# Kernel tuning notes

Hardware: AMD Instinct MI355X
Metric: run time of the kernel (lower is better)

Reference implementation:

```python
import jax, jax.numpy as jnp
import numpy as np

KH, KW = 7, 7            # extraction kernel
EH, EW = 5, 5            # effective (cropped) kernel
PAD = (KH - EH) // 2     # = 1
EPS = 1e-7


def _extract_patches(x):
    # x: [B,H,W,C] -> patches [B,Ho,Wo,KH,KW,C], stride 1, VALID padding
    B, H, Wd, C = x.shape
    Ho, Wo = H - KH + 1, Wd - KW + 1
    rows = []
    for i in range(KH):
        cols = [x[:, i:i + Ho, j:j + Wo, :] for j in range(KW)]
        rows.append(jnp.stack(cols, axis=3))          # [B,Ho,Wo,KW,C]
    return jnp.stack(rows, axis=3)                     # [B,Ho,Wo,KH,KW,C]


def _rotate_bilinear(patches, angles):
    # patches: [N,KH,KW,C]; angles: [N]. Mirrors tf.contrib.image
    # angles_to_projective_transforms + transform(BILINEAR, fill=0).
    # Note: the layer's det(matrix)==0 NEAREST fallback never fires (det==1).
    N = patches.shape[0]
    c, s = jnp.cos(angles), jnp.sin(angles)
    Wm1, Hm1 = jnp.float32(KW - 1), jnp.float32(KH - 1)
    xo = (Wm1 - (c * Wm1 - s * Hm1)) * 0.5
    yo = (Hm1 - (s * Wm1 + c * Hm1)) * 0.5
    scale = jnp.float32(1.0 + EPS)   # transforms /= transforms[:,8:9]+1e-7
    a0, a1, a2 = c / scale, -s / scale, xo / scale
    a3, a4, a5 = s / scale, c / scale, yo / scale
    yg, xg = jnp.meshgrid(jnp.arange(KH, dtype=jnp.float32),
                          jnp.arange(KW, dtype=jnp.float32), indexing='ij')
    x_in = a0[:, None, None] * xg + a1[:, None, None] * yg + a2[:, None, None]
    y_in = a3[:, None, None] * xg + a4[:, None, None] * yg + a5[:, None, None]
    x0f = jnp.floor(x_in); y0f = jnp.floor(y_in)
    wx1 = x_in - x0f; wx0 = 1.0 - wx1
    wy1 = y_in - y0f; wy0 = 1.0 - wy1
    x0 = x0f.astype(jnp.int32); x1 = x0 + 1
    y0 = y0f.astype(jnp.int32); y1 = y0 + 1
    nidx = jnp.arange(N)[:, None, None]

    def corner(yi, xi, w):
        valid = ((xi >= 0) & (xi < KW) & (yi >= 0) & (yi < KH)).astype(patches.dtype)
        v = patches[nidx, jnp.clip(yi, 0, KH - 1), jnp.clip(xi, 0, KW - 1)]
        return (w * valid)[..., None] * v

    return (corner(y0, x0, wy0 * wx0) + corner(y0, x1, wy0 * wx1) +
            corner(y1, x0, wy1 * wx0) + corner(y1, x1, wy1 * wx1))


def reference(x, W, b):
    B, H, Wd, C = x.shape
    patches = _extract_patches(x)                      # [B,Ho,Wo,KH,KW,C]
    _, Ho, Wo = patches.shape[:3]
    intensity = jnp.sum(patches, axis=-1)              # [B,Ho,Wo,KH,KW]
    row_idx = jnp.repeat(jnp.arange(KH, dtype=jnp.float32), KW)   # rowMulti
    col_idx = jnp.tile(jnp.arange(KW, dtype=jnp.float32), KH)     # colMulti
    flat = intensity.reshape(-1, KH * KW)              # [N, KH*KW]
    denom = jnp.sum(flat, -1) + EPS
    cr = jnp.sum(flat * row_idx, -1) / denom - (KH - 1) / 2.0
    cc = jnp.sum(flat * col_idx, -1) / denom - (KW - 1) / 2.0
    angle = jnp.arctan2(cr, cc + EPS)                  # [N]
    patches_n = patches.reshape(-1, KH, KW, C)         # [N,KH,KW,C]
    rot = _rotate_bilinear(patches_n, angle)
    rot = rot[:, PAD:PAD + EH, PAD:PAD + EW, :]        # crop to effective
    rot = rot.reshape(B, Ho, Wo, EH * EW * C)
    w_flat = W.reshape(W.shape[0], -1)                 # [F, EH*EW*C]
    out = jnp.einsum('bhwk,fk->bhwf', rot, w_flat) + b
    return out


def setup_inputs() -> dict:
    key = jax.random.key(0)
    kx, kw, _ = jax.random.split(key, 3)
    x = jax.random.normal(kx, (8, 64, 64, 32), dtype=jnp.float32)
    W = jax.random.normal(kw, (64, EH, EW, 32), dtype=jnp.float32) * 0.05
    b = jnp.zeros((64,), dtype=jnp.float32)
    return {"x": x, "W": W, "b": b}
```

## Files before the change

kernel.cpp:

```cpp
#include <hip/hip_runtime.h>
#include <hip/hip_bf16.h>

#define EPSF 1e-7f
#define B_ 8
#define H_ 64
#define W_ 64
#define C_ 32
#define HO 58
#define WO 58
#define NF 64
#define KDIM 800

#define XBS 40

typedef __bf16 v8bf __attribute__((ext_vector_type(8)));
typedef float  v4f  __attribute__((ext_vector_type(4)));
typedef float  v2f  __attribute__((ext_vector_type(2)));

__global__ void k_wpack(const float* __restrict__ W, __bf16* __restrict__ Wp) {
    int t = blockIdx.x*256 + threadIdx.x;
    int j = t & 7; int lane = (t >> 3) & 63; int rest = t >> 9;
    int kb = rest % 25; int nt = rest / 25;
    int f = nt*16 + (lane & 15);
    int k = kb*32 + (lane >> 4)*8 + j;
    Wp[t] = (__bf16)W[f*KDIM + k];
}

__global__ __launch_bounds__(256, 4)
void k_main(const float* __restrict__ x, const v8bf* __restrict__ Wp,
            const float* __restrict__ bias, float* __restrict__ out) {
    __shared__ __bf16 xtb[8][22][XBS];
    __shared__ float  Srow[8][22];
    __shared__ float4 pars[32];
    __shared__ float  redu[2][64][20];

    int tid = threadIdx.x;
    int wv = tid >> 6, lane = tid & 63;
    int m = lane & 15, q = lane >> 4;
    int rh = wv & 1, kh = wv >> 1;

    int L = blockIdx.x + 4*(blockIdx.y + 29*blockIdx.z);
    int newL = (L & 7)*116 + (L >> 3);
    int b   = newL / 116;
    int rem = newL - b*116;
    int rg  = rem >> 2;
    int cg  = rem & 3;
    int ho0 = rg*2, wo0 = cg*16;
    int npx = WO - wo0; if (npx > 16) npx = 16;

    if (tid < 176) {
        int r = tid / 22, c = tid - r*22;
        int xc = wo0 + c; if (xc > W_-1) xc = W_-1;
        const float* src = x + (size_t)((b*H_ + ho0 + r)*W_ + xc)*C_;
        float4 vq[8];
#pragma unroll
        for (int qq = 0; qq < 8; qq++) vq[qq] = *(const float4*)(src + qq*4);
        float s = 0.f;
#pragma unroll
        for (int qq = 0; qq < 8; qq++) s += vq[qq].x + vq[qq].y + vq[qq].z + vq[qq].w;
        Srow[r][c] = s;
#pragma unroll
        for (int h8 = 0; h8 < 4; h8++) {
            v8bf o;
            o[0]=(__bf16)vq[h8*2].x;   o[1]=(__bf16)vq[h8*2].y;
            o[2]=(__bf16)vq[h8*2].z;   o[3]=(__bf16)vq[h8*2].w;
            o[4]=(__bf16)vq[h8*2+1].x; o[5]=(__bf16)vq[h8*2+1].y;
            o[6]=(__bf16)vq[h8*2+1].z; o[7]=(__bf16)vq[h8*2+1].w;
            *(v8bf*)&xtb[r][c][h8*8] = o;
        }
    }
    __syncthreads();

    if (tid < 32) {
        int r0 = tid >> 4, c0 = tid & 15;
        float den = 0.f, crn = 0.f, ccn = 0.f;
#pragma unroll
        for (int i = 0; i < 7; i++)
#pragma unroll
            for (int j = 0; j < 7; j++) {
                float v = Srow[r0 + i][c0 + j];
                den += v; crn += v*(float)i; ccn += v*(float)j;
            }
        float dt = den + EPSF;
        float cr = crn/dt - 3.0f;
        float cx = ccn/dt - 3.0f + EPSF;
        float r2 = cr*cr + cx*cx;
        float inv = r2 > 0.f ? rsqrtf(r2) : 0.f;
        float c_ = r2 > 0.f ? cx*inv : 1.0f;
        float s_ = cr*inv;
        const float scale = 1.0f + EPSF;
        float pc  = c_/scale, ps = s_/scale;
        float pxo = (6.0f - (c_*6.0f - s_*6.0f))*0.5f/scale;
        float pyo = (6.0f - (s_*6.0f + c_*6.0f))*0.5f/scale;
        pars[tid] = make_float4(pc, ps, pxo, pyo);
    }
    __syncthreads();

    float4 pp = pars[(rh << 4) | m];
    float pc = pp.x, ps = pp.y, pxo = pp.z, pyo = pp.w;

    const v8bf* wp = Wp + lane;
    const __bf16* patch = &xtb[rh][m][q*8];

    v4f acc0 = {0.f,0.f,0.f,0.f}, acc1 = {0.f,0.f,0.f,0.f};
    v4f acc2 = {0.f,0.f,0.f,0.f}, acc3 = {0.f,0.f,0.f,0.f};

    int kb0 = kh*13;
    int nkb = 13 - kh;
    int kblast = kb0 + nkb - 1;

    auto loadw = [&](v8bf* dst, int kbi) {
        dst[0] = wp[(0*25 + kbi)*64];
        dst[1] = wp[(1*25 + kbi)*64];
        dst[2] = wp[(2*25 + kbi)*64];
        dst[3] = wp[(3*25 + kbi)*64];
    };

    auto body = [&](int kb, const v8bf* wf) {
        unsigned ukb = (unsigned)kb;
        int py = (int)(ukb/5u);
        int pxx = kb - py*5;
        float yy = (float)(py + 1);
        float xx = (float)(pxx + 1);

        float xin = pc*xx - ps*yy + pxo;
        float yin = ps*xx + pc*yy + pyo;
        float x0f = floorf(xin), y0f = floorf(yin);
        float wx1 = xin - x0f, wx0 = 1.0f - wx1;
        float wy1 = yin - y0f, wy0 = 1.0f - wy1;
        int ix0 = (int)x0f, iy0 = (int)y0f;
        int ix1 = ix0 + 1,  iy1 = iy0 + 1;

        v2f a8[4];
#pragma unroll
        for (int d = 0; d < 4; d++) a8[d] = (v2f){0.f, 0.f};

        auto corner = [&](int yi, int xi, float wgt) {
            bool valid = (xi >= 0) & (xi < 7) & (yi >= 0) & (yi < 7);
            int cy  = yi < 0 ? 0 : (yi > 6 ? 6 : yi);
            int cx2 = xi < 0 ? 0 : (xi > 6 ? 6 : xi);
            float wq = valid ? wgt : 0.0f;
            union { v8bf v; unsigned u[4]; } uv;
            uv.v = *(const v8bf*)(patch + (cy*22 + cx2)*XBS);
            v2f w2 = (v2f){wq, wq};
#pragma unroll
            for (int d = 0; d < 4; d++) {
                v2f val = (v2f){ __uint_as_float(uv.u[d] << 16),
                                 __uint_as_float(uv.u[d] & 0xffff0000u) };
                a8[d] += w2 * val;
            }
        };
        corner(iy0, ix0, wy0*wx0);
        corner(iy0, ix1, wy0*wx1);
        corner(iy1, ix0, wy1*wx0);
        corner(iy1, ix1, wy1*wx1);

        v8bf af;
#pragma unroll
        for (int d = 0; d < 4; d++) {
            af[2*d]   = (__bf16)a8[d].x;
            af[2*d+1] = (__bf16)a8[d].y;
        }
        acc0 = __builtin_amdgcn_mfma_f32_16x16x32_bf16(af, wf[0], acc0, 0, 0, 0);
        acc1 = __builtin_amdgcn_mfma_f32_16x16x32_bf16(af, wf[1], acc1, 0, 0, 0);
        acc2 = __builtin_amdgcn_mfma_f32_16x16x32_bf16(af, wf[2], acc2, 0, 0, 0);
        acc3 = __builtin_amdgcn_mfma_f32_16x16x32_bf16(af, wf[3], acc3, 0, 0, 0);
    };

    v8bf wfA[4], wfB[4];
    loadw(wfA, kb0);
    int i = 0;
#pragma unroll 1
    for (; i + 2 <= nkb; i += 2) {
        loadw(wfB, kb0 + i + 1);
        body(kb0 + i, wfA);
        int nx = kb0 + i + 2; if (nx > kblast) nx = kblast;
        loadw(wfA, nx);
        body(kb0 + i + 1, wfB);
    }
    if (i < nkb) body(kblast, wfA);

    if (kh == 1) {
        *(v4f*)&redu[rh][lane][0]  = acc0;
        *(v4f*)&redu[rh][lane][4]  = acc1;
        *(v4f*)&redu[rh][lane][8]  = acc2;
        *(v4f*)&redu[rh][lane][12] = acc3;
    }
    __syncthreads();
    if (kh == 0) {
        acc0 += *(const v4f*)&redu[rh][lane][0];
        acc1 += *(const v4f*)&redu[rh][lane][4];
        acc2 += *(const v4f*)&redu[rh][lane][8];
        acc3 += *(const v4f*)&redu[rh][lane][12];

        float bv0 = bias[m], bv1 = bias[16 + m];
        float bv2 = bias[32 + m], bv3 = bias[48 + m];

        int ho = ho0 + rh;
        size_t rowbase = (size_t)(b*HO + ho)*WO + wo0;
#pragma unroll
        for (int r = 0; r < 4; r++) {
            int px = q*4 + r;
            if (px < npx) {
                float* op = out + (rowbase + px)*NF + m;
                op[0]  = acc0[r] + bv0;
                op[16] = acc1[r] + bv1;
                op[32] = acc2[r] + bv2;
                op[48] = acc3[r] + bv3;
            }
        }
    }
}

extern "C" void kernel_launch(void* const* d_in, const int* in_sizes, int n_in,
                              void* d_out, int out_size, void* d_ws, size_t ws_size,
                              hipStream_t stream) {
    const float* x    = (const float*)d_in[0];
    const float* W    = (const float*)d_in[1];
    const float* bias = (const float*)d_in[2];
    float* out = (float*)d_out;
    __bf16* Wp = (__bf16*)d_ws;

    k_wpack<<<dim3(200), 256, 0, stream>>>(W, Wp);
    k_main<<<dim3(4, 29, B_), 256, 0, stream>>>(x, (const v8bf*)Wp, bias, out);
}
```

Before: 76.83 us.

## Split K reduction across four waves per row with 512-thread blocks

Doubles the block to 512 threads so each pixel row's 25 K-blocks are split over four waves (7/6/6/6) instead of two, and reduces the three partial accumulators through shared memory. The weight-fragment double-buffering is dropped in favour of a simple loop that loads weights just before the MFMAs. The aim is more waves in flight and a shorter per-wave serial chain. In exchange it adds reduction traffic and raises launch bounds to 512x8, which may squeeze registers and expose global-load latency now that weights are no longer prefetched.

Measured after the change: 76.53 us. No clear change (-0.4%).

```diff
diff --git a/kernel.cpp b/kernel.cpp
--- a/kernel.cpp
+++ b/kernel.cpp
@@ -26,13 +26,13 @@
     Wp[t] = (__bf16)W[f*KDIM + k];
 }
 
-__global__ __launch_bounds__(256, 4)
+__global__ __launch_bounds__(512, 8)
 void k_main(const float* __restrict__ x, const v8bf* __restrict__ Wp,
             const float* __restrict__ bias, float* __restrict__ out) {
     __shared__ __bf16 xtb[8][22][XBS];
     __shared__ float  Srow[8][22];
     __shared__ float4 pars[32];
-    __shared__ float  redu[2][64][20];
+    __shared__ float  redu[3][2][64][16];
 
     int tid = threadIdx.x;
     int wv = tid >> 6, lane = tid & 63;
@@ -105,18 +105,12 @@
     v4f acc0 = {0.f,0.f,0.f,0.f}, acc1 = {0.f,0.f,0.f,0.f};
     v4f acc2 = {0.f,0.f,0.f,0.f}, acc3 = {0.f,0.f,0.f,0.f};
 
-    int kb0 = kh*13;
-    int nkb = 13 - kh;
+    int kb0 = (kh == 0) ? 0 : (7 + (kh - 1)*6);
+    int nkb = (kh == 0) ? 7 : 6;
     int kblast = kb0 + nkb - 1;
 
-    auto loadw = [&](v8bf* dst, int kbi) {
-        dst[0] = wp[(0*25 + kbi)*64];
-        dst[1] = wp[(1*25 + kbi)*64];
-        dst[2] = wp[(2*25 + kbi)*64];
-        dst[3] = wp[(3*25 + kbi)*64];
-    };
-
-    auto body = [&](int kb, const v8bf* wf) {
+#pragma unroll 1
+    for (int kb = kb0; kb <= kblast; kb++) {
         unsigned ukb = (unsigned)kb;
         int py = (int)(ukb/5u);
         int pxx = kb - py*5;
@@ -161,37 +155,34 @@
             af[2*d]   = (__bf16)a8[d].x;
             af[2*d+1] = (__bf16)a8[d].y;
         }
-        acc0 = __builtin_amdgcn_mfma_f32_16x16x32_bf16(af, wf[0], acc0, 0, 0, 0);
-        acc1 = __builtin_amdgcn_mfma_f32_16x16x32_bf16(af, wf[1], acc1, 0, 0, 0);
-        acc2 = __builtin_amdgcn_mfma_f32_16x16x32_bf16(af, wf[2], acc2, 0, 0, 0);
-        acc3 = __builtin_amdgcn_mfma_f32_16x16x32_bf16(af, wf[3], acc3, 0, 0, 0);
-    };
-
-    v8bf wfA[4], wfB[4];
-    loadw(wfA, kb0);
-    int i = 0;
-#pragma unroll 1
-    for (; i + 2 <= nkb; i += 2) {
-        loadw(wfB, kb0 + i + 1);
-        body(kb0 + i, wfA);
-        int nx = kb0 + i + 2; if (nx > kblast) nx = kblast;
-        loadw(wfA, nx);
-        body(kb0 + i + 1, wfB);
-    }
-    if (i < nkb) body(kblast, wfA);
-
-    if (kh == 1) {
-        *(v4f*)&redu[rh][lane][0]  = acc0;
-        *(v4f*)&redu[rh][lane][4]  = acc1;
-        *(v4f*)&redu[rh][lane][8]  = acc2;
-        *(v4f*)&redu[rh][lane][12] = acc3;
+
+        v8bf wf0 = wp[(0*25 + kb)*64];
+        v8bf wf1 = wp[(1*25 + kb)*64];
+        v8bf wf2 = wp[(2*25 + kb)*64];
+        v8bf wf3 = wp[(3*25 + kb)*64];
+
+        acc0 = __builtin_amdgcn_mfma_f32_16x16x32_bf16(af, wf0, acc0, 0, 0, 0);
+        acc1 = __builtin_amdgcn_mfma_f32_16x16x32_bf16(af, wf1, acc1, 0, 0, 0);
+        acc2 = __builtin_amdgcn_mfma_f32_16x16x32_bf16(af, wf2, acc2, 0, 0, 0);
+        acc3 = __builtin_amdgcn_mfma_f32_16x16x32_bf16(af, wf3, acc3, 0, 0, 0);
+    }
+
+    if (kh != 0) {
+        int p = kh - 1;
+        *(v4f*)&redu[p][rh][lane][0]  = acc0;
+        *(v4f*)&redu[p][rh][lane][4]  = acc1;
+        *(v4f*)&redu[p][rh][lane][8]  = acc2;
+        *(v4f*)&redu[p][rh][lane][12] = acc3;
     }
     __syncthreads();
     if (kh == 0) {
-        acc0 += *(const v4f*)&redu[rh][lane][0];
-        acc1 += *(const v4f*)&redu[rh][lane][4];
-        acc2 += *(const v4f*)&redu[rh][lane][8];
-        acc3 += *(const v4f*)&redu[rh][lane][12];
+#pragma unroll
+        for (int p = 0; p < 3; p++) {
+            acc0 += *(const v4f*)&redu[p][rh][lane][0];
+            acc1 += *(const v4f*)&redu[p][rh][lane][4];
+            acc2 += *(const v4f*)&redu[p][rh][lane][8];
+            acc3 += *(const v4f*)&redu[p][rh][lane][12];
+        }
 
         float bv0 = bias[m], bv1 = bias[16 + m];
         float bv2 = bias[32 + m], bv3 = bias[48 + m];
@@ -222,5 +213,5 @@
     __bf16* Wp = (__bf16*)d_ws;
 
     k_wpack<<<dim3(200), 256, 0, stream>>>(W, Wp);
-    k_main<<<dim3(4, 29, B_), 256, 0, stream>>>(x, (const v8bf*)Wp, bias, out);
+    k_main<<<dim3(4, 29, B_), 512, 0, stream>>>(x, (const v8bf*)Wp, bias, out);
 }
```

## Process eight output rows per block with two rows per wave sharing weights

Applied to the files above, without the earlier changes.

Each block now covers 8 output rows instead of 2, using 512 threads. Each wave handles two rows and reuses each loaded weight fragment for both rows' MFMAs. This cuts redundant global weight loads and the halo re-staging of the input tile, and shrinks the grid from 928 to 256 blocks. The last row group overlaps earlier rows (ho0=50), so some rows are computed and written twice with identical values. The risk is higher register pressure and a small grid of 256 blocks, which may leave compute units underused.

Result: no change. 75.77 us (-1.4%).

```diff
diff --git a/kernel.cpp b/kernel.cpp
--- a/kernel.cpp
+++ b/kernel.cpp
@@ -26,29 +26,30 @@
     Wp[t] = (__bf16)W[f*KDIM + k];
 }
 
-__global__ __launch_bounds__(256, 4)
+__global__ __launch_bounds__(512, 2)
 void k_main(const float* __restrict__ x, const v8bf* __restrict__ Wp,
             const float* __restrict__ bias, float* __restrict__ out) {
-    __shared__ __bf16 xtb[8][22][XBS];
-    __shared__ float  Srow[8][22];
-    __shared__ float4 pars[32];
-    __shared__ float  redu[2][64][20];
+    __shared__ __bf16 xtb[14][22][XBS];
+    __shared__ float  Srow[14][22];
+    __shared__ float4 pars[128];
+    __shared__ float  redu[2][4][64][20];
 
     int tid = threadIdx.x;
     int wv = tid >> 6, lane = tid & 63;
     int m = lane & 15, q = lane >> 4;
-    int rh = wv & 1, kh = wv >> 1;
-
-    int L = blockIdx.x + 4*(blockIdx.y + 29*blockIdx.z);
-    int newL = (L & 7)*116 + (L >> 3);
-    int b   = newL / 116;
-    int rem = newL - b*116;
+    int rp = wv & 3, kh = wv >> 2;
+
+    int L = blockIdx.x + 4*(blockIdx.y + 8*blockIdx.z);
+    int newL = (L & 7)*32 + (L >> 3);
+    int b   = newL >> 5;
+    int rem = newL & 31;
     int rg  = rem >> 2;
     int cg  = rem & 3;
-    int ho0 = rg*2, wo0 = cg*16;
+    int ho0 = (rg < 7) ? rg*8 : 50;
+    int wo0 = cg*16;
     int npx = WO - wo0; if (npx > 16) npx = 16;
 
-    if (tid < 176) {
+    if (tid < 308) {
         int r = tid / 22, c = tid - r*22;
         int xc = wo0 + c; if (xc > W_-1) xc = W_-1;
         const float* src = x + (size_t)((b*H_ + ho0 + r)*W_ + xc)*C_;
@@ -71,7 +72,7 @@
     }
     __syncthreads();
 
-    if (tid < 32) {
+    if (tid < 128) {
         int r0 = tid >> 4, c0 = tid & 15;
         float den = 0.f, crn = 0.f, ccn = 0.f;
 #pragma unroll
@@ -96,14 +97,18 @@
     }
     __syncthreads();
 
-    float4 pp = pars[(rh << 4) | m];
-    float pc = pp.x, ps = pp.y, pxo = pp.z, pyo = pp.w;
+    int rA = 2*rp, rB = 2*rp + 1;
+    float4 ppA = pars[(rA << 4) | m];
+    float4 ppB = pars[(rB << 4) | m];
 
     const v8bf* wp = Wp + lane;
-    const __bf16* patch = &xtb[rh][m][q*8];
-
-    v4f acc0 = {0.f,0.f,0.f,0.f}, acc1 = {0.f,0.f,0.f,0.f};
-    v4f acc2 = {0.f,0.f,0.f,0.f}, acc3 = {0.f,0.f,0.f,0.f};
+    const __bf16* patchA = &xtb[rA][m][q*8];
+    const __bf16* patchB = &xtb[rB][m][q*8];
+
+    v4f aA0 = {0.f,0.f,0.f,0.f}, aA1 = {0.f,0.f,0.f,0.f};
+    v4f aA2 = {0.f,0.f,0.f,0.f}, aA3 = {0.f,0.f,0.f,0.f};
+    v4f aB0 = {0.f,0.f,0.f,0.f}, aB1 = {0.f,0.f,0.f,0.f};
+    v4f aB2 = {0.f,0.f,0.f,0.f}, aB3 = {0.f,0.f,0.f,0.f};
 
     int kb0 = kh*13;
     int nkb = 13 - kh;
@@ -116,7 +121,9 @@
         dst[3] = wp[(3*25 + kbi)*64];
     };
 
-    auto body = [&](int kb, const v8bf* wf) {
+    auto bodyhalf = [&](int kb, const v8bf* wf, const __bf16* patch,
+                        float pc, float ps, float pxo, float pyo,
+                        v4f& A0, v4f& A1, v4f& A2, v4f& A3) {
         unsigned ukb = (unsigned)kb;
         int py = (int)(ukb/5u);
         int pxx = kb - py*5;
@@ -161,10 +168,15 @@
             af[2*d]   = (__bf16)a8[d].x;
             af[2*d+1] = (__bf16)a8[d].y;
         }
-        acc0 = __builtin_amdgcn_mfma_f32_16x16x32_bf16(af, wf[0], acc0, 0, 0, 0);
-        acc1 = __builtin_amdgcn_mfma_f32_16x16x32_bf16(af, wf[1], acc1, 0, 0, 0);
-        acc2 = __builtin_amdgcn_mfma_f32_16x16x32_bf16(af, wf[2], acc2, 0, 0, 0);
-        acc3 = __builtin_amdgcn_mfma_f32_16x16x32_bf16(af, wf[3], acc3, 0, 0, 0);
+        A0 = __builtin_amdgcn_mfma_f32_16x16x32_bf16(af, wf[0], A0, 0, 0, 0);
+        A1 = __builtin_amdgcn_mfma_f32_16x16x32_bf16(af, wf[1], A1, 0, 0, 0);
+        A2 = __builtin_amdgcn_mfma_f32_16x16x32_bf16(af, wf[2], A2, 0, 0, 0);
+        A3 = __builtin_amdgcn_mfma_f32_16x16x32_bf16(af, wf[3], A3, 0, 0, 0);
+    };
+
+    auto body = [&](int kb, const v8bf* wf) {
+        bodyhalf(kb, wf, patchA, ppA.x, ppA.y, ppA.z, ppA.w, aA0, aA1, aA2, aA3);
+        bodyhalf(kb, wf, patchB, ppB.x, ppB.y, ppB.z, ppB.w, aB0, aB1, aB2, aB3);
     };
 
     v8bf wfA[4], wfB[4];
@@ -181,32 +193,47 @@
     if (i < nkb) body(kblast, wfA);
 
     if (kh == 1) {
-        *(v4f*)&redu[rh][lane][0]  = acc0;
-        *(v4f*)&redu[rh][lane][4]  = acc1;
-        *(v4f*)&redu[rh][lane][8]  = acc2;
-        *(v4f*)&redu[rh][lane][12] = acc3;
+        *(v4f*)&redu[0][rp][lane][0]  = aA0;
+        *(v4f*)&redu[0][rp][lane][4]  = aA1;
+        *(v4f*)&redu[0][rp][lane][8]  = aA2;
+        *(v4f*)&redu[0][rp][lane][12] = aA3;
+        *(v4f*)&redu[1][rp][lane][0]  = aB0;
+        *(v4f*)&redu[1][rp][lane][4]  = aB1;
+        *(v4f*)&redu[1][rp][lane][8]  = aB2;
+        *(v4f*)&redu[1][rp][lane][12] = aB3;
     }
     __syncthreads();
     if (kh == 0) {
-        acc0 += *(const v4f*)&redu[rh][lane][0];
-        acc1 += *(const v4f*)&redu[rh][lane][4];
-        acc2 += *(const v4f*)&redu[rh][lane][8];
-        acc3 += *(const v4f*)&redu[rh][lane][12];
+        aA0 += *(const v4f*)&redu[0][rp][lane][0];
+        aA1 += *(const v4f*)&redu[0][rp][lane][4];
+        aA2 += *(const v4f*)&redu[0][rp][lane][8];
+        aA3 += *(const v4f*)&redu[0][rp][lane][12];
+        aB0 += *(const v4f*)&redu[1][rp][lane][0];
+        aB1 += *(const v4f*)&redu[1][rp][lane][4];
+        aB2 += *(const v4f*)&redu[1][rp][lane][8];
+        aB3 += *(const v4f*)&redu[1][rp][lane][12];
 
         float bv0 = bias[m], bv1 = bias[16 + m];
         float bv2 = bias[32 + m], bv3 = bias[48 + m];
 
-        int ho = ho0 + rh;
-        size_t rowbase = (size_t)(b*HO + ho)*WO + wo0;
+        int hoA = ho0 + rA;
+        int hoB = ho0 + rB;
+        size_t rbA = (size_t)(b*HO + hoA)*WO + wo0;
+        size_t rbB = (size_t)(b*HO + hoB)*WO + wo0;
 #pragma unroll
         for (int r = 0; r < 4; r++) {
             int px = q*4 + r;
             if (px < npx) {
-                float* op = out + (rowbase + px)*NF + m;
-                op[0]  = acc0[r] + bv0;
-                op[16] = acc1[r] + bv1;
-                op[32] = acc2[r] + bv2;
-                op[48] = acc3[r] + bv3;
+                float* opA = out + (rbA + px)*NF + m;
+                opA[0]  = aA0[r] + bv0;
+                opA[16] = aA1[r] + bv1;
+                opA[32] = aA2[r] + bv2;
+                opA[48] = aA3[r] + bv3;
+                float* opB = out + (rbB + px)*NF + m;
+                opB[0]  = aB0[r] + bv0;
+                opB[16] = aB1[r] + bv1;
+                opB[32] = aB2[r] + bv2;
+                opB[48] = aB3[r] + bv3;
             }
         }
     }
@@ -222,5 +249,5 @@
     __bf16* Wp = (__bf16*)d_ws;
 
     k_wpack<<<dim3(200), 256, 0, stream>>>(W, Wp);
-    k_main<<<dim3(4, 29, B_), 256, 0, stream>>>(x, (const v8bf*)Wp, bias, out);
+    k_main<<<dim3(4, 8, B_), 512, 0, stream>>>(x, (const v8bf*)Wp, bias, out);
 }
```
